# Performance work log

Measured on AMD Instinct MI355X. Metric: run time of the kernel, lower is better.

Reference implementation:

```python
import jax, jax.numpy as jnp
import numpy as np

N, T, J, NB = 2048, 81, 16, 15
D_ATT, HEADS, SEQ, D_LIN, NOISE = 48, 6, 31, 256, 45
BN_EPS, LN_EPS, SLOPE = 1e-5, 1e-6, 0.01

# Human3.6M 16-joint skeleton bone (parent, child) pairs
_BONES = [(0,1),(1,2),(2,3),(0,4),(4,5),(5,6),(0,7),(7,8),(8,9),(9,10),(8,11),(11,12),(12,13),(8,14),(14,15)]
BONES_P = np.array([p for p, c in _BONES])
BONES_C = np.array([c for p, c in _BONES])
_parent = {c: p for p, c in _BONES}
_bone_of = {c: i for i, (p, c) in enumerate(_BONES)}
_M = np.zeros((NB, J), np.float32)  # M[i,j]=1 iff bone i lies on root->joint j chain
for j in range(1, J):
    jj = j
    while jj != 0:
        _M[_bone_of[jj], j] = 1.0
        jj = _parent[jj]
M_BONE2POSE = jnp.asarray(_M)
FIXED_MASK = jnp.ones((NB,), jnp.float32).at[jnp.array([6, 7])].set(0.0)  # torso bones kept fixed


def _layer_norm(t, a, b):
    mean = t.mean(-1, keepdims=True)
    # torch.std default is unbiased (ddof=1); module divides by (std + eps)
    std = jnp.sqrt(((t - mean) ** 2).sum(-1, keepdims=True) / (t.shape[-1] - 1))
    return a * (t - mean) / (std + LN_EPS) + b


def _leaky(x):
    return jnp.where(x >= 0, x, SLOPE * x)


def _axis_angle_to_matrix(v):
    # Rodrigues: v (..., 3) axis-angle -> (..., 3, 3)
    theta = jnp.linalg.norm(v, axis=-1, keepdims=True)
    k = v / jnp.maximum(theta, 1e-8)
    c = jnp.cos(theta)[..., None]
    s = jnp.sin(theta)[..., None]
    kx, ky, kz = k[..., 0], k[..., 1], k[..., 2]
    z = jnp.zeros_like(kx)
    K = jnp.stack([jnp.stack([z, -kz, ky], -1),
                   jnp.stack([kz, z, -kx], -1),
                   jnp.stack([-ky, kx, z], -1)], -2)
    kk = k[..., :, None] * k[..., None, :]
    return c * jnp.eye(3, dtype=v.dtype) + s * K + (1 - c) * kk


def setup_inputs() -> dict:
    key = jax.random.key(0)
    ks = jax.random.split(key, 12)
    w = lambda k, shape, scale=0.05: jax.random.normal(k, shape, jnp.float32) * scale
    return {
        'inputs_3d': jax.random.normal(ks[0], (N, 1, T, J, 3), jnp.float32),
        'noise': jax.random.normal(ks[1], (N, NOISE), jnp.float32),
        'enc_w': w(ks[2], (D_ATT, 3)), 'enc_b': jnp.zeros((D_ATT,), jnp.float32),
        'enc_bn_g': jnp.ones((D_ATT,), jnp.float32), 'enc_bn_b': jnp.zeros((D_ATT,), jnp.float32),
        'ln_a': jnp.ones((D_ATT,), jnp.float32), 'ln_b': jnp.zeros((D_ATT,), jnp.float32),
        'wq': w(ks[3], (D_ATT, D_ATT)), 'bq': jnp.zeros((D_ATT,), jnp.float32),
        'wk': w(ks[4], (D_ATT, D_ATT)), 'bk': jnp.zeros((D_ATT,), jnp.float32),
        'wv': w(ks[5], (D_ATT, D_ATT)), 'bv': jnp.zeros((D_ATT,), jnp.float32),
        'wo': w(ks[6], (D_ATT, D_ATT)), 'bo': jnp.zeros((D_ATT,), jnp.float32),
        'w1': w(ks[7], (D_LIN, SEQ * D_ATT)), 'b1': jnp.zeros((D_LIN,), jnp.float32),
        'bn1_g': jnp.ones((D_LIN,), jnp.float32), 'bn1_b': jnp.zeros((D_LIN,), jnp.float32),
        'w2': w(ks[8], (NB * 4, D_LIN)), 'b2': w(ks[9], (NB * 4,), 0.1),
    }


def reference(inputs_3d, noise, enc_w, enc_b, enc_bn_g, enc_bn_b, ln_a, ln_b,
              wq, bq, wk, bk, wv, bv, wo, bo, w1, b1, bn1_g, bn1_b, w2, b2):
    x5 = inputs_3d[:, 0]                                  # (n, T, 16, 3)
    root = x5[:, :, :1, :]
    x = x5 - root                                         # root-centered
    bvec = x[..., BONES_C, :] - x[..., BONES_P, :]        # (n, T, 15, 3)
    blen = jnp.linalg.norm(bvec, axis=-1, keepdims=True)
    bunit = bvec / blen
    n, t_len = x.shape[0], x.shape[1]
    mid = (t_len - 1) // 2

    x_ = x[:, mid].reshape(n, -1)                         # (n, 48)
    y = jnp.concatenate([x_, noise], axis=-1).reshape(n, SEQ, 3)
    # Conv1d(k=1) == per-token linear; BatchNorm eval (running mean 0, var 1); Dropout off
    y = jax.nn.relu((y @ enc_w.T + enc_b) * enc_bn_g / jnp.sqrt(1.0 + BN_EPS) + enc_bn_b)

    # tiny 6-head self-attention with pre-LayerNorm and residual
    h = _layer_norm(y, ln_a, ln_b)
    d = D_ATT // HEADS
    q = (h @ wq.T + bq).reshape(n, SEQ, HEADS, d).transpose(0, 2, 1, 3)
    k = (h @ wk.T + bk).reshape(n, SEQ, HEADS, d).transpose(0, 2, 1, 3)
    v = (h @ wv.T + bv).reshape(n, SEQ, HEADS, d).transpose(0, 2, 1, 3)
    probs = jax.nn.softmax(jnp.einsum('nhqd,nhkd->nhqk', q, k) / (d ** 0.5), axis=-1)
    ctx = jnp.einsum('nhqk,nhkd->nhqd', probs, v).transpose(0, 2, 1, 3).reshape(n, SEQ, D_ATT)
    y = y + (ctx @ wo.T + bo)

    y = y.reshape(n, -1)                                  # (n, 1488)
    y = _leaky((y @ w1.T + b1) * bn1_g / jnp.sqrt(1.0 + BN_EPS) + bn1_b)
    y = _leaky(y @ w2.T + b2).reshape(n, NB, 4)           # (n, 15, 4)

    axis = y[..., :3]
    axis = axis / jnp.linalg.norm(axis, axis=-1, keepdims=True)
    theta = y[..., 3:4] / t_len                           # (n, 15, 1)
    t_idx = jnp.arange(t_len, dtype=y.dtype)              # (T,)
    vaa = axis[:, None] * (theta[:, None] * t_idx[None, :, None, None])  # (n, T, 15, 3)
    R = _axis_angle_to_matrix(vaa)                        # (n, T, 15, 3, 3)
    mod_unit = jnp.einsum('ntbij,ntbj->ntbi', R, bunit)
    mask = FIXED_MASK[None, None, :, None]
    mod_unit = mod_unit * mask + bunit * (1 - mask)
    ba_diff = 1 - jnp.sum(mod_unit * bunit, axis=-1)      # (n, T, 15)
    mod_bone = mod_unit * blen
    out = jnp.einsum('ntbc,bj->ntjc', mod_bone, M_BONE2POSE) + root  # (n, T, 16, 3)
    return out, ba_diff
```

## Files before the change

### kernel.cpp

```cpp
#include <hip/hip_runtime.h>
#include <math.h>

#define NS   2048
#define TL   81
#define NBN  15
#define DA   48
#define SQL  31
#define KD   1488
#define DL   256
#define MID  40

#define INV_SQRT_BN 0.99999500003749969f
#define SCALE_ATT   0.35355339059327373f

__global__ __launch_bounds__(256)
void attn_kernel(const float* __restrict__ x5, const float* __restrict__ noise,
                 const float* __restrict__ enc_w, const float* __restrict__ enc_b,
                 const float* __restrict__ enc_g, const float* __restrict__ enc_bb,
                 const float* __restrict__ ln_a, const float* __restrict__ ln_b,
                 const float* __restrict__ wq, const float* __restrict__ bq,
                 const float* __restrict__ wk, const float* __restrict__ bk,
                 const float* __restrict__ wv, const float* __restrict__ bv,
                 const float* __restrict__ wo, const float* __restrict__ bo,
                 float* __restrict__ y2)
{
    __shared__ float s93[96];
    __shared__ float sy[32*49];
    __shared__ float sh[32*49];
    __shared__ float sW[3*48*49];
    __shared__ __align__(16) float sQKV[32*148];
    __shared__ float smean[32], sinv[32];

    const int tid = threadIdx.x;
    const int n = blockIdx.x;

    if (tid < 93) {
        float v;
        if (tid < 48) {
            const float* base = x5 + ((size_t)n*TL + MID)*48;
            v = base[tid] - base[tid % 3];
        } else {
            v = noise[(size_t)n*45 + (tid-48)];
        }
        s93[tid] = v;
    }
    #pragma unroll
    for (int l=0; l<9; l++){
        int idx = tid + l*256;
        int f = idx/48, c = idx - f*48;
        int o = f*49 + c;
        sW[o]        = wq[idx];
        sW[2352 + o] = wk[idx];
        sW[4704 + o] = wv[idx];
    }
    __syncthreads();

    for (int idx=tid; idx<SQL*DA; idx+=256){
        int s = idx/48, f = idx - s*48;
        float a = enc_b[f]
                + s93[s*3+0]*enc_w[f*3+0]
                + s93[s*3+1]*enc_w[f*3+1]
                + s93[s*3+2]*enc_w[f*3+2];
        float v = a * (enc_g[f]*INV_SQRT_BN) + enc_bb[f];
        sy[s*49+f] = fmaxf(v, 0.0f);
    }
    __syncthreads();

    if (tid < SQL){
        float m = 0.f;
        for (int f=0; f<48; f++) m += sy[tid*49+f];
        m *= (1.0f/48.0f);
        float vs = 0.f;
        for (int f=0; f<48; f++){ float d = sy[tid*49+f]-m; vs += d*d; }
        float sd = sqrtf(vs * (1.0f/47.0f));
        smean[tid] = m;
        sinv[tid]  = 1.0f/(sd + 1e-6f);
    }
    __syncthreads();

    for (int idx=tid; idx<SQL*DA; idx+=256){
        int s = idx/48, f = idx - s*48;
        sh[s*49+f] = ln_a[f]*(sy[s*49+f]-smean[s])*sinv[s] + ln_b[f];
    }
    __syncthreads();

    if (tid < 192){
        const int sg = tid/24, fg = tid - (tid/24)*24;
        const int arr = fg >> 3;
        const int f0  = (fg & 7)*6;
        const float* wb = sW + arr*2352 + f0*49;
        const float* hb = sh + sg*4*49;
        float a0[6]={0,0,0,0,0,0}, a1[6]={0,0,0,0,0,0};
        float a2[6]={0,0,0,0,0,0}, a3[6]={0,0,0,0,0,0};
        for (int c=0; c<48; c++){
            float h0 = hb[c], h1 = hb[49+c], h2 = hb[98+c], h3 = hb[147+c];
            #pragma unroll
            for (int i=0;i<6;i++){
                float w = wb[i*49+c];
                a0[i] += h0*w; a1[i] += h1*w; a2[i] += h2*w; a3[i] += h3*w;
            }
        }
        const float* bias = (arr==0)? bq : (arr==1? bk : bv);
        #pragma unroll
        for (int i=0;i<6;i++){
            float b = bias[f0+i];
            int col = arr*48 + f0 + i;
            sQKV[(sg*4+0)*148 + col] = a0[i] + b;
            sQKV[(sg*4+1)*148 + col] = a1[i] + b;
            sQKV[(sg*4+2)*148 + col] = a2[i] + b;
            sQKV[(sg*4+3)*148 + col] = a3[i] + b;
        }
    }
    __syncthreads();

    #pragma unroll
    for (int l=0; l<9; l++){
        int idx = tid + l*256;
        sW[(idx/48)*49 + (idx%48)] = wo[idx];
    }
    if (tid < 186){
        const int hd = tid/31, qi = tid - (tid/31)*31;
        const float4 q0 = *(const float4*)(sQKV + qi*148 + hd*8);
        const float4 q1 = *(const float4*)(sQKV + qi*148 + hd*8 + 4);
        float sc[31]; float mx = -1e30f;
        for (int ki=0; ki<31; ki++){
            const float4 k0 = *(const float4*)(sQKV + ki*148 + 48 + hd*8);
            const float4 k1 = *(const float4*)(sQKV + ki*148 + 48 + hd*8 + 4);
            float d = q0.x*k0.x + q0.y*k0.y + q0.z*k0.z + q0.w*k0.w
                    + q1.x*k1.x + q1.y*k1.y + q1.z*k1.z + q1.w*k1.w;
            d *= SCALE_ATT;
            sc[ki] = d; mx = fmaxf(mx, d);
        }
        float ssum = 0.f;
        for (int ki=0; ki<31; ki++){ float e = expf(sc[ki]-mx); sc[ki]=e; ssum += e; }
        float rin = 1.0f/ssum;
        float4 c0 = {0,0,0,0}, c1 = {0,0,0,0};
        for (int ki=0; ki<31; ki++){
            float p = sc[ki];
            const float4 v0 = *(const float4*)(sQKV + ki*148 + 96 + hd*8);
            const float4 v1 = *(const float4*)(sQKV + ki*148 + 96 + hd*8 + 4);
            c0.x += p*v0.x; c0.y += p*v0.y; c0.z += p*v0.z; c0.w += p*v0.w;
            c1.x += p*v1.x; c1.y += p*v1.y; c1.z += p*v1.z; c1.w += p*v1.w;
        }
        float* cb = sh + qi*49 + hd*8;
        cb[0]=c0.x*rin; cb[1]=c0.y*rin; cb[2]=c0.z*rin; cb[3]=c0.w*rin;
        cb[4]=c1.x*rin; cb[5]=c1.y*rin; cb[6]=c1.z*rin; cb[7]=c1.w*rin;
    }
    __syncthreads();

    if (tid < 192){
        const int sg = tid/12, fg = tid - (tid/12)*12;
        const int f0 = fg*4;
        const float* wb = sW + f0*49;
        const float* cb = sh + sg*2*49;
        float a0[4]={0,0,0,0}, a1[4]={0,0,0,0};
        for (int c=0; c<48; c++){
            float x0 = cb[c], x1 = cb[49+c];
            #pragma unroll
            for (int i=0;i<4;i++){
                float w = wb[i*49+c];
                a0[i] += x0*w; a1[i] += x1*w;
            }
        }
        {
            int s = sg*2;
            if (s < 31){
                float* dst = y2 + (size_t)n*KD + s*48 + f0;
                const float* yb = sy + s*49 + f0;
                #pragma unroll
                for (int i=0;i<4;i++) dst[i] = yb[i] + a0[i] + bo[f0+i];
            }
        }
        {
            int s = sg*2+1;
            if (s < 31){
                float* dst = y2 + (size_t)n*KD + s*48 + f0;
                const float* yb = sy + s*49 + f0;
                #pragma unroll
                for (int i=0;i<4;i++) dst[i] = yb[i] + a1[i] + bo[f0+i];
            }
        }
    }
}

#define KSP 6
#define KPS 248
#define KCH 8

__global__ __launch_bounds__(256)
void gemm1_kernel(const float* __restrict__ y2, const float* __restrict__ w1,
                  float* __restrict__ y3raw, int use_partial)
{
    __shared__ __align__(16) float sB[KCH*256];
    __shared__ __align__(16) float sA[KCH*20];
    const int tid = threadIdx.x;
    const int bx = blockIdx.x;
    const int m0 = (bx & 127) * 16;
    const int split = bx >> 7;
    const int ks0 = split * KPS;
    const int c0 = (tid & 15)*4 + (tid >> 6)*64;
    const int r0 = ((tid >> 4) & 3)*4;

    const int bn = tid >> 1;
    const int bg = (tid & 1)*4;
    const int ar = tid >> 1;
    const int ag = (tid & 1)*4;

    float acc[4][4];
    #pragma unroll
    for (int i=0;i<4;i++)
        #pragma unroll
        for (int j=0;j<4;j++) acc[i][j]=0.f;

    for (int ch=0; ch<31; ch++){
        const int k0 = ks0 + ch*KCH;
        float4 b0v = *(const float4*)(w1 + (size_t)bn*KD        + k0 + bg);
        float4 b1v = *(const float4*)(w1 + (size_t)(bn+128)*KD  + k0 + bg);
        float4 av;
        if (tid < 32) av = *(const float4*)(y2 + (size_t)(m0+ar)*KD + k0 + ag);
        __syncthreads();
        sB[(bg+0)*256 + bn] = b0v.x;  sB[(bg+1)*256 + bn] = b0v.y;
        sB[(bg+2)*256 + bn] = b0v.z;  sB[(bg+3)*256 + bn] = b0v.w;
        sB[(bg+0)*256 + bn+128] = b1v.x;  sB[(bg+1)*256 + bn+128] = b1v.y;
        sB[(bg+2)*256 + bn+128] = b1v.z;  sB[(bg+3)*256 + bn+128] = b1v.w;
        if (tid < 32){
            sA[(ag+0)*20 + ar] = av.x;  sA[(ag+1)*20 + ar] = av.y;
            sA[(ag+2)*20 + ar] = av.z;  sA[(ag+3)*20 + ar] = av.w;
        }
        __syncthreads();
        #pragma unroll
        for (int kk=0; kk<KCH; kk++){
            float4 b = *(const float4*)(sB + kk*256 + c0);
            float4 a = *(const float4*)(sA + kk*20 + r0);
            acc[0][0] += a.x*b.x; acc[0][1] += a.x*b.y; acc[0][2] += a.x*b.z; acc[0][3] += a.x*b.w;
            acc[1][0] += a.y*b.x; acc[1][1] += a.y*b.y; acc[1][2] += a.y*b.z; acc[1][3] += a.y*b.w;
            acc[2][0] += a.z*b.x; acc[2][1] += a.z*b.y; acc[2][2] += a.z*b.z; acc[2][3] += a.z*b.w;
            acc[3][0] += a.w*b.x; acc[3][1] += a.w*b.y; acc[3][2] += a.w*b.z; acc[3][3] += a.w*b.w;
        }
    }

    if (use_partial){
        float* dst = y3raw + (size_t)split*NS*DL;
        #pragma unroll
        for (int i=0;i<4;i++){
            float4 v; v.x=acc[i][0]; v.y=acc[i][1]; v.z=acc[i][2]; v.w=acc[i][3];
            *(float4*)(dst + (size_t)(m0+r0+i)*DL + c0) = v;
        }
    } else {
        #pragma unroll
        for (int i=0;i<4;i++)
            #pragma unroll
            for (int j=0;j<4;j++)
                atomicAdd(y3raw + (size_t)(m0+r0+i)*DL + c0 + j, acc[i][j]);
    }
}

__global__ __launch_bounds__(256)
void head_kernel(const float* __restrict__ y3raw, const float* __restrict__ w2,
                 const float* __restrict__ b2, const float* __restrict__ b1,
                 const float* __restrict__ g1, const float* __restrict__ bb1,
                 float* __restrict__ at, int nsl)
{
    __shared__ float swc[64*60];
    __shared__ __align__(16) float sy3[16*256];
    __shared__ float sy4[16*61];
    const int tid = threadIdx.x;
    const int n0 = blockIdx.x * 16;

    #pragma unroll
    for (int l=0;l<4;l++){
        int idx = tid + l*256;
        int s = idx >> 6, i4 = (idx & 63) << 2;
        const float* src = y3raw + (size_t)(n0+s)*256 + i4;
        float4 v = *(const float4*)(src);
        if (nsl == 6){
            #pragma unroll
            for (int sl=1; sl<6; sl++){
                float4 p = *(const float4*)(src + (size_t)sl*NS*DL);
                v.x += p.x; v.y += p.y; v.z += p.z; v.w += p.w;
            }
        }
        const float4 vb = *(const float4*)(b1 + i4);
        const float4 vg = *(const float4*)(g1 + i4);
        const float4 vs = *(const float4*)(bb1 + i4);
        v.x = (v.x + vb.x)*(vg.x*INV_SQRT_BN) + vs.x;  v.x = v.x>=0.f? v.x : 0.01f*v.x;
        v.y = (v.y + vb.y)*(vg.y*INV_SQRT_BN) + vs.y;  v.y = v.y>=0.f? v.y : 0.01f*v.y;
        v.z = (v.z + vb.z)*(vg.z*INV_SQRT_BN) + vs.z;  v.z = v.z>=0.f? v.z : 0.01f*v.z;
        v.w = (v.w + vb.w)*(vg.w*INV_SQRT_BN) + vs.w;  v.w = v.w>=0.f? v.w : 0.01f*v.w;
        *(float4*)(sy3 + s*256 + i4) = v;
    }

    float acc[4]; int ss[4], mm[4];
    #pragma unroll
    for (int l=0;l<4;l++){
        int uu = tid + l*256;
        ss[l]=0; mm[l]=0; acc[l]=0.f;
        if (uu < 960){ ss[l]=uu/60; mm[l]=uu-ss[l]*60; acc[l]=b2[mm[l]]; }
    }

    for (int ch=0; ch<4; ch++){
        const int i0 = ch*64;
        __syncthreads();
        #pragma unroll
        for (int l=0;l<15;l++){
            int idx = tid + l*256;
            int m = idx >> 6, io = idx & 63;
            swc[io*60 + m] = w2[(size_t)m*256 + i0 + io];
        }
        __syncthreads();
        #pragma unroll
        for (int l=0;l<4;l++){
            int uu = tid + l*256;
            if (uu < 960){
                const float* yy = sy3 + ss[l]*256 + i0;
                float a = acc[l];
                #pragma unroll 8
                for (int io=0; io<64; io++) a += yy[io]*swc[io*60 + mm[l]];
                acc[l] = a;
            }
        }
    }
    __syncthreads();
    #pragma unroll
    for (int l=0;l<4;l++){
        int uu = tid + l*256;
        if (uu < 960){
            float a = acc[l];
            sy4[ss[l]*61 + mm[l]] = a>=0.f? a : 0.01f*a;
        }
    }
    __syncthreads();
    if (tid < 240){
        int s = tid/15, b = tid - s*15;
        const float* y4 = sy4 + s*61 + b*4;
        float ax=y4[0], ay=y4[1], az=y4[2], th=y4[3];
        float nr = sqrtf(ax*ax+ay*ay+az*az);
        float4 o;
        o.x = ax/nr; o.y = ay/nr; o.z = az/nr; o.w = th/81.0f;
        *(float4*)(at + (size_t)(n0+s)*60 + b*4) = o;
    }
}

__global__ __launch_bounds__(256)
void pose_kernel(const float* __restrict__ x5, const float* __restrict__ at,
                 float* __restrict__ out)
{
    const int gid = blockIdx.x*256 + threadIdx.x;
    if (gid >= NS*TL) return;
    const int n = gid / TL;
    const int t = gid - n*TL;
    const float ft = (float)t;

    float4 pv[12];
    {
        const float4* src = (const float4*)(x5 + (size_t)gid*48);
        #pragma unroll
        for (int i=0;i<12;i++) pv[i] = src[i];
    }
    float* p = (float*)pv;
    const float4* ab = (const float4*)(at + (size_t)n*60);

    float4 posv[12];
    float* pos = (float*)posv;
    pos[0]=p[0]; pos[1]=p[1]; pos[2]=p[2];
    float ba[15];

    const int PJ[15] = {0,1,2,0,4,5,0,7,8,9,8,11,12,8,14};
    const int CJ[15] = {1,2,3,4,5,6,7,8,9,10,11,12,13,14,15};

    #pragma unroll
    for (int b=0;b<15;b++){
        const int pj = PJ[b], cj = CJ[b];
        float bx = p[cj*3+0]-p[pj*3+0];
        float by = p[cj*3+1]-p[pj*3+1];
        float bz = p[cj*3+2]-p[pj*3+2];
        float bl = sqrtf(bx*bx+by*by+bz*bz);
        float ux = bx/bl, uy = by/bl, uz = bz/bl;
        float mx, my, mz;
        if (b==6 || b==7){
            mx=ux; my=uy; mz=uz;
        } else {
            float4 a = ab[b];
            float ang = a.w * ft;
            float cs = cosf(ang), sn = sinf(ang);
            float kd = a.x*ux + a.y*uy + a.z*uz;
            float cx = a.y*uz - a.z*uy;
            float cy = a.z*ux - a.x*uz;
            float cz = a.x*uy - a.y*ux;
            float oc = (1.0f-cs)*kd;
            mx = ux*cs + cx*sn + a.x*oc;
            my = uy*cs + cy*sn + a.y*oc;
            mz = uz*cs + cz*sn + a.z*oc;
        }
        ba[b] = 1.0f - (mx*ux+my*uy+mz*uz);
        pos[cj*3+0] = pos[pj*3+0] + mx*bl;
        pos[cj*3+1] = pos[pj*3+1] + my*bl;
        pos[cj*3+2] = pos[pj*3+2] + mz*bl;
    }

    {
        float4* dst = (float4*)(out + (size_t)gid*48);
        #pragma unroll
        for (int i=0;i<12;i++) dst[i] = posv[i];
    }
    {
        float* bd = out + (size_t)NS*TL*48 + (size_t)gid*15;
        #pragma unroll
        for (int b=0;b<15;b++) bd[b] = ba[b];
    }
}

extern "C" void kernel_launch(void* const* d_in, const int* in_sizes, int n_in,
                              void* d_out, int out_size, void* d_ws, size_t ws_size,
                              hipStream_t stream)
{
    const float* x5    = (const float*)d_in[0];
    const float* noise = (const float*)d_in[1];
    const float* enc_w = (const float*)d_in[2];
    const float* enc_b = (const float*)d_in[3];
    const float* enc_g = (const float*)d_in[4];
    const float* enc_bb= (const float*)d_in[5];
    const float* ln_a  = (const float*)d_in[6];
    const float* ln_b  = (const float*)d_in[7];
    const float* wq = (const float*)d_in[8];
    const float* bq = (const float*)d_in[9];
    const float* wk = (const float*)d_in[10];
    const float* bk = (const float*)d_in[11];
    const float* wv = (const float*)d_in[12];
    const float* bv = (const float*)d_in[13];
    const float* wo = (const float*)d_in[14];
    const float* bo = (const float*)d_in[15];
    const float* w1 = (const float*)d_in[16];
    const float* b1 = (const float*)d_in[17];
    const float* g1 = (const float*)d_in[18];
    const float* bb1= (const float*)d_in[19];
    const float* w2 = (const float*)d_in[20];
    const float* b2 = (const float*)d_in[21];
    float* out = (float*)d_out;

    float* ws = (float*)d_ws;
    float* y2 = ws;
    float* y3 = y2 + (size_t)NS*KD;

    const size_t need_partial = ((size_t)NS*KD + 6*(size_t)NS*DL + (size_t)NS*60) * 4;
    const int use_partial = (ws_size >= need_partial) ? 1 : 0;
    const int nsl = use_partial ? 6 : 1;
    float* at = y3 + (size_t)nsl*NS*DL;

    if (!use_partial)
        hipMemsetAsync(y3, 0, (size_t)NS*DL*sizeof(float), stream);

    attn_kernel<<<NS, 256, 0, stream>>>(x5, noise, enc_w, enc_b, enc_g, enc_bb,
                                        ln_a, ln_b, wq,bq,wk,bk,wv,bv,wo,bo, y2);
    gemm1_kernel<<<128*KSP, 256, 0, stream>>>(y2, w1, y3, use_partial);
    head_kernel<<<128, 256, 0, stream>>>(y3, w2, b2, b1, g1, bb1, at, nsl);
    pose_kernel<<<(NS*TL+255)/256, 256, 0, stream>>>(x5, at, out);

    (void)in_sizes; (void)n_in; (void)out_size;
}
```

Baseline: 252.2 us.

## Restructure attention kernel to one thread per token, reuse output buffer for partials

Rewrites the attention stage so each thread owns one sequence token, with two samples per 64-thread block. Encoding, layer norm and the Q/K/V/O projections now stay in registers, and only per-head K/V go through shared memory. Weights are read directly from global memory through the cache instead of being staged in shared memory. The split-K partial sums of the first GEMM are now always written into the output buffer as scratch, which drops the atomic fallback and the memset. The per-thread register arrays (y, h, o with 48 floats each) raise register pressure and may cause spills or low occupancy.

```diff
diff --git a/kernel.cpp b/kernel.cpp
--- a/kernel.cpp
+++ b/kernel.cpp
@@ -13,7 +13,7 @@
 #define INV_SQRT_BN 0.99999500003749969f
 #define SCALE_ATT   0.35355339059327373f
 
-__global__ __launch_bounds__(256)
+__global__ __launch_bounds__(64)
 void attn_kernel(const float* __restrict__ x5, const float* __restrict__ noise,
                  const float* __restrict__ enc_w, const float* __restrict__ enc_b,
                  const float* __restrict__ enc_g, const float* __restrict__ enc_bb,
@@ -24,161 +24,144 @@
                  const float* __restrict__ wo, const float* __restrict__ bo,
                  float* __restrict__ y2)
 {
-    __shared__ float s93[96];
-    __shared__ float sy[32*49];
-    __shared__ float sh[32*49];
-    __shared__ float sW[3*48*49];
-    __shared__ __align__(16) float sQKV[32*148];
-    __shared__ float smean[32], sinv[32];
-
-    const int tid = threadIdx.x;
-    const int n = blockIdx.x;
-
-    if (tid < 93) {
-        float v;
-        if (tid < 48) {
-            const float* base = x5 + ((size_t)n*TL + MID)*48;
-            v = base[tid] - base[tid % 3];
-        } else {
-            v = noise[(size_t)n*45 + (tid-48)];
-        }
-        s93[tid] = v;
-    }
-    #pragma unroll
-    for (int l=0; l<9; l++){
-        int idx = tid + l*256;
-        int f = idx/48, c = idx - f*48;
-        int o = f*49 + c;
-        sW[o]        = wq[idx];
-        sW[2352 + o] = wk[idx];
-        sW[4704 + o] = wv[idx];
-    }
-    __syncthreads();
-
-    for (int idx=tid; idx<SQL*DA; idx+=256){
-        int s = idx/48, f = idx - s*48;
-        float a = enc_b[f]
-                + s93[s*3+0]*enc_w[f*3+0]
-                + s93[s*3+1]*enc_w[f*3+1]
-                + s93[s*3+2]*enc_w[f*3+2];
-        float v = a * (enc_g[f]*INV_SQRT_BN) + enc_bb[f];
-        sy[s*49+f] = fmaxf(v, 0.0f);
-    }
-    __syncthreads();
-
-    if (tid < SQL){
-        float m = 0.f;
-        for (int f=0; f<48; f++) m += sy[tid*49+f];
-        m *= (1.0f/48.0f);
-        float vs = 0.f;
-        for (int f=0; f<48; f++){ float d = sy[tid*49+f]-m; vs += d*d; }
-        float sd = sqrtf(vs * (1.0f/47.0f));
-        smean[tid] = m;
-        sinv[tid]  = 1.0f/(sd + 1e-6f);
-    }
-    __syncthreads();
-
-    for (int idx=tid; idx<SQL*DA; idx+=256){
-        int s = idx/48, f = idx - s*48;
-        sh[s*49+f] = ln_a[f]*(sy[s*49+f]-smean[s])*sinv[s] + ln_b[f];
-    }
-    __syncthreads();
-
-    if (tid < 192){
-        const int sg = tid/24, fg = tid - (tid/24)*24;
-        const int arr = fg >> 3;
-        const int f0  = (fg & 7)*6;
-        const float* wb = sW + arr*2352 + f0*49;
-        const float* hb = sh + sg*4*49;
-        float a0[6]={0,0,0,0,0,0}, a1[6]={0,0,0,0,0,0};
-        float a2[6]={0,0,0,0,0,0}, a3[6]={0,0,0,0,0,0};
-        for (int c=0; c<48; c++){
-            float h0 = hb[c], h1 = hb[49+c], h2 = hb[98+c], h3 = hb[147+c];
+    __shared__ __align__(16) float sK[2*32*12];
+    __shared__ __align__(16) float sV[2*32*12];
+
+    const int lane = threadIdx.x;
+    const int smp  = lane >> 5;
+    const int s    = lane & 31;
+    const int scl  = (s < 31) ? s : 30;
+    const int n    = blockIdx.x*2 + smp;
+
+    float x0, x1, x2;
+    if (scl < 16){
+        const float* base = x5 + ((size_t)n*TL + MID)*48;
+        x0 = base[scl*3+0] - base[0];
+        x1 = base[scl*3+1] - base[1];
+        x2 = base[scl*3+2] - base[2];
+    } else {
+        const float* nb = noise + (size_t)n*45 + (scl*3 - 48);
+        x0 = nb[0]; x1 = nb[1]; x2 = nb[2];
+    }
+
+    float y[48];
+    #pragma unroll
+    for (int f=0; f<48; f++){
+        float a = enc_b[f] + x0*enc_w[f*3+0] + x1*enc_w[f*3+1] + x2*enc_w[f*3+2];
+        float v = a*(enc_g[f]*INV_SQRT_BN) + enc_bb[f];
+        y[f] = fmaxf(v, 0.0f);
+    }
+
+    float mean = 0.f;
+    #pragma unroll
+    for (int f=0; f<48; f++) mean += y[f];
+    mean *= (1.0f/48.0f);
+    float vs = 0.f;
+    #pragma unroll
+    for (int f=0; f<48; f++){ float d = y[f]-mean; vs += d*d; }
+    const float rstd = 1.0f/(sqrtf(vs*(1.0f/47.0f)) + 1e-6f);
+    float h[48];
+    #pragma unroll
+    for (int f=0; f<48; f++) h[f] = ln_a[f]*(y[f]-mean)*rstd + ln_b[f];
+
+    float o[48];
+    #pragma unroll
+    for (int f=0; f<48; f++) o[f] = 0.f;
+
+    #pragma unroll 1
+    for (int hd=0; hd<6; hd++){
+        const float* wqh = wq + hd*8*48;
+        const float* wkh = wk + hd*8*48;
+        const float* wvh = wv + hd*8*48;
+        float q8[8], k8[8], v8[8];
+        #pragma unroll
+        for (int j=0; j<8; j++){
+            q8[j] = bq[hd*8+j]; k8[j] = bk[hd*8+j]; v8[j] = bv[hd*8+j];
+        }
+        #pragma unroll
+        for (int j=0; j<8; j++){
+            const float* wqr = wqh + j*48;
+            const float* wkr = wkh + j*48;
+            const float* wvr = wvh + j*48;
+            float aq = q8[j], ak = k8[j], av = v8[j];
             #pragma unroll
-            for (int i=0;i<6;i++){
-                float w = wb[i*49+c];
-                a0[i] += h0*w; a1[i] += h1*w; a2[i] += h2*w; a3[i] += h3*w;
+            for (int c=0; c<48; c++){
+                float hc = h[c];
+                aq += hc*wqr[c];
+                ak += hc*wkr[c];
+                av += hc*wvr[c];
             }
-        }
-        const float* bias = (arr==0)? bq : (arr==1? bk : bv);
-        #pragma unroll
-        for (int i=0;i<6;i++){
-            float b = bias[f0+i];
-            int col = arr*48 + f0 + i;
-            sQKV[(sg*4+0)*148 + col] = a0[i] + b;
-            sQKV[(sg*4+1)*148 + col] = a1[i] + b;
-            sQKV[(sg*4+2)*148 + col] = a2[i] + b;
-            sQKV[(sg*4+3)*148 + col] = a3[i] + b;
-        }
-    }
-    __syncthreads();
-
-    #pragma unroll
-    for (int l=0; l<9; l++){
-        int idx = tid + l*256;
-        sW[(idx/48)*49 + (idx%48)] = wo[idx];
-    }
-    if (tid < 186){
-        const int hd = tid/31, qi = tid - (tid/31)*31;
-        const float4 q0 = *(const float4*)(sQKV + qi*148 + hd*8);
-        const float4 q1 = *(const float4*)(sQKV + qi*148 + hd*8 + 4);
-        float sc[31]; float mx = -1e30f;
+            q8[j] = aq; k8[j] = ak; v8[j] = av;
+        }
+
+        float* kr = sK + (smp*32+s)*12;
+        float* vr = sV + (smp*32+s)*12;
+        float4 t0, t1;
+        t0.x=k8[0]; t0.y=k8[1]; t0.z=k8[2]; t0.w=k8[3];
+        t1.x=k8[4]; t1.y=k8[5]; t1.z=k8[6]; t1.w=k8[7];
+        *(float4*)(kr) = t0; *(float4*)(kr+4) = t1;
+        t0.x=v8[0]; t0.y=v8[1]; t0.z=v8[2]; t0.w=v8[3];
+        t1.x=v8[4]; t1.y=v8[5]; t1.z=v8[6]; t1.w=v8[7];
+        *(float4*)(vr) = t0; *(float4*)(vr+4) = t1;
+        __syncthreads();
+
+        float sc[31];
+        float mx = -1e30f;
+        #pragma unroll
         for (int ki=0; ki<31; ki++){
-            const float4 k0 = *(const float4*)(sQKV + ki*148 + 48 + hd*8);
-            const float4 k1 = *(const float4*)(sQKV + ki*148 + 48 + hd*8 + 4);
-            float d = q0.x*k0.x + q0.y*k0.y + q0.z*k0.z + q0.w*k0.w
-                    + q1.x*k1.x + q1.y*k1.y + q1.z*k1.z + q1.w*k1.w;
+            const float* kp = sK + (smp*32+ki)*12;
+            float4 ka = *(const float4*)(kp);
+            float4 kb = *(const float4*)(kp+4);
+            float d = q8[0]*ka.x + q8[1]*ka.y + q8[2]*ka.z + q8[3]*ka.w
+                    + q8[4]*kb.x + q8[5]*kb.y + q8[6]*kb.z + q8[7]*kb.w;
             d *= SCALE_ATT;
-            sc[ki] = d; mx = fmaxf(mx, d);
+            sc[ki] = d;
+            mx = fmaxf(mx, d);
         }
         float ssum = 0.f;
-        for (int ki=0; ki<31; ki++){ float e = expf(sc[ki]-mx); sc[ki]=e; ssum += e; }
-        float rin = 1.0f/ssum;
-        float4 c0 = {0,0,0,0}, c1 = {0,0,0,0};
+        #pragma unroll
         for (int ki=0; ki<31; ki++){
+            float e = __expf(sc[ki]-mx);
+            sc[ki] = e; ssum += e;
+        }
+        const float rin = 1.0f/ssum;
+
+        float c8[8];
+        #pragma unroll
+        for (int j=0; j<8; j++) c8[j] = 0.f;
+        #pragma unroll
+        for (int ki=0; ki<31; ki++){
+            const float* vp = sV + (smp*32+ki)*12;
+            float4 va = *(const float4*)(vp);
+            float4 vb = *(const float4*)(vp+4);
             float p = sc[ki];
-            const float4 v0 = *(const float4*)(sQKV + ki*148 + 96 + hd*8);
-            const float4 v1 = *(const float4*)(sQKV + ki*148 + 96 + hd*8 + 4);
-            c0.x += p*v0.x; c0.y += p*v0.y; c0.z += p*v0.z; c0.w += p*v0.w;
-            c1.x += p*v1.x; c1.y += p*v1.y; c1.z += p*v1.z; c1.w += p*v1.w;
-        }
-        float* cb = sh + qi*49 + hd*8;
-        cb[0]=c0.x*rin; cb[1]=c0.y*rin; cb[2]=c0.z*rin; cb[3]=c0.w*rin;
-        cb[4]=c1.x*rin; cb[5]=c1.y*rin; cb[6]=c1.z*rin; cb[7]=c1.w*rin;
-    }
-    __syncthreads();
-
-    if (tid < 192){
-        const int sg = tid/12, fg = tid - (tid/12)*12;
-        const int f0 = fg*4;
-        const float* wb = sW + f0*49;
-        const float* cb = sh + sg*2*49;
-        float a0[4]={0,0,0,0}, a1[4]={0,0,0,0};
-        for (int c=0; c<48; c++){
-            float x0 = cb[c], x1 = cb[49+c];
+            c8[0] += p*va.x; c8[1] += p*va.y; c8[2] += p*va.z; c8[3] += p*va.w;
+            c8[4] += p*vb.x; c8[5] += p*vb.y; c8[6] += p*vb.z; c8[7] += p*vb.w;
+        }
+        #pragma unroll
+        for (int j=0; j<8; j++) c8[j] *= rin;
+
+        #pragma unroll
+        for (int f=0; f<48; f++){
+            const float* wor = wo + f*48 + hd*8;
+            float a = o[f];
             #pragma unroll
-            for (int i=0;i<4;i++){
-                float w = wb[i*49+c];
-                a0[i] += x0*w; a1[i] += x1*w;
-            }
-        }
-        {
-            int s = sg*2;
-            if (s < 31){
-                float* dst = y2 + (size_t)n*KD + s*48 + f0;
-                const float* yb = sy + s*49 + f0;
-                #pragma unroll
-                for (int i=0;i<4;i++) dst[i] = yb[i] + a0[i] + bo[f0+i];
-            }
-        }
-        {
-            int s = sg*2+1;
-            if (s < 31){
-                float* dst = y2 + (size_t)n*KD + s*48 + f0;
-                const float* yb = sy + s*49 + f0;
-                #pragma unroll
-                for (int i=0;i<4;i++) dst[i] = yb[i] + a1[i] + bo[f0+i];
-            }
+            for (int j=0; j<8; j++) a += c8[j]*wor[j];
+            o[f] = a;
+        }
+        __syncthreads();
+    }
+
+    if (s < 31){
+        float* dst = y2 + (size_t)n*KD + s*48;
+        #pragma unroll
+        for (int f4=0; f4<12; f4++){
+            float4 v;
+            v.x = y[f4*4+0] + o[f4*4+0] + bo[f4*4+0];
+            v.y = y[f4*4+1] + o[f4*4+1] + bo[f4*4+1];
+            v.z = y[f4*4+2] + o[f4*4+2] + bo[f4*4+2];
+            v.w = y[f4*4+3] + o[f4*4+3] + bo[f4*4+3];
+            *(float4*)(dst + f4*4) = v;
         }
     }
 }
@@ -189,7 +172,7 @@
 
 __global__ __launch_bounds__(256)
 void gemm1_kernel(const float* __restrict__ y2, const float* __restrict__ w1,
-                  float* __restrict__ y3raw, int use_partial)
+                  float* __restrict__ y3p)
 {
     __shared__ __align__(16) float sB[KCH*256];
     __shared__ __align__(16) float sA[KCH*20];
@@ -239,27 +222,19 @@
         }
     }
 
-    if (use_partial){
-        float* dst = y3raw + (size_t)split*NS*DL;
-        #pragma unroll
-        for (int i=0;i<4;i++){
-            float4 v; v.x=acc[i][0]; v.y=acc[i][1]; v.z=acc[i][2]; v.w=acc[i][3];
-            *(float4*)(dst + (size_t)(m0+r0+i)*DL + c0) = v;
-        }
-    } else {
-        #pragma unroll
-        for (int i=0;i<4;i++)
-            #pragma unroll
-            for (int j=0;j<4;j++)
-                atomicAdd(y3raw + (size_t)(m0+r0+i)*DL + c0 + j, acc[i][j]);
+    float* dst = y3p + (size_t)split*NS*DL;
+    #pragma unroll
+    for (int i=0;i<4;i++){
+        float4 v; v.x=acc[i][0]; v.y=acc[i][1]; v.z=acc[i][2]; v.w=acc[i][3];
+        *(float4*)(dst + (size_t)(m0+r0+i)*DL + c0) = v;
     }
 }
 
 __global__ __launch_bounds__(256)
-void head_kernel(const float* __restrict__ y3raw, const float* __restrict__ w2,
+void head_kernel(const float* __restrict__ y3p, const float* __restrict__ w2,
                  const float* __restrict__ b2, const float* __restrict__ b1,
                  const float* __restrict__ g1, const float* __restrict__ bb1,
-                 float* __restrict__ at, int nsl)
+                 float* __restrict__ at)
 {
     __shared__ float swc[64*60];
     __shared__ __align__(16) float sy3[16*256];
@@ -271,22 +246,20 @@
     for (int l=0;l<4;l++){
         int idx = tid + l*256;
         int s = idx >> 6, i4 = (idx & 63) << 2;
-        const float* src = y3raw + (size_t)(n0+s)*256 + i4;
+        const float* src = y3p + (size_t)(n0+s)*256 + i4;
         float4 v = *(const float4*)(src);
-        if (nsl == 6){
-            #pragma unroll
-            for (int sl=1; sl<6; sl++){
-                float4 p = *(const float4*)(src + (size_t)sl*NS*DL);
-                v.x += p.x; v.y += p.y; v.z += p.z; v.w += p.w;
-            }
+        #pragma unroll
+        for (int sl=1; sl<6; sl++){
+            float4 p = *(const float4*)(src + (size_t)sl*NS*DL);
+            v.x += p.x; v.y += p.y; v.z += p.z; v.w += p.w;
         }
         const float4 vb = *(const float4*)(b1 + i4);
         const float4 vg = *(const float4*)(g1 + i4);
-        const float4 vs = *(const float4*)(bb1 + i4);
-        v.x = (v.x + vb.x)*(vg.x*INV_SQRT_BN) + vs.x;  v.x = v.x>=0.f? v.x : 0.01f*v.x;
-        v.y = (v.y + vb.y)*(vg.y*INV_SQRT_BN) + vs.y;  v.y = v.y>=0.f? v.y : 0.01f*v.y;
-        v.z = (v.z + vb.z)*(vg.z*INV_SQRT_BN) + vs.z;  v.z = v.z>=0.f? v.z : 0.01f*v.z;
-        v.w = (v.w + vb.w)*(vg.w*INV_SQRT_BN) + vs.w;  v.w = v.w>=0.f? v.w : 0.01f*v.w;
+        const float4 vsb = *(const float4*)(bb1 + i4);
+        v.x = (v.x + vb.x)*(vg.x*INV_SQRT_BN) + vsb.x;  v.x = v.x>=0.f? v.x : 0.01f*v.x;
+        v.y = (v.y + vb.y)*(vg.y*INV_SQRT_BN) + vsb.y;  v.y = v.y>=0.f? v.y : 0.01f*v.y;
+        v.z = (v.z + vb.z)*(vg.z*INV_SQRT_BN) + vsb.z;  v.z = v.z>=0.f? v.z : 0.01f*v.z;
+        v.w = (v.w + vb.w)*(vg.w*INV_SQRT_BN) + vsb.w;  v.w = v.w>=0.f? v.w : 0.01f*v.w;
         *(float4*)(sy3 + s*256 + i4) = v;
     }
 
@@ -440,21 +413,14 @@
 
     float* ws = (float*)d_ws;
     float* y2 = ws;
-    float* y3 = y2 + (size_t)NS*KD;
-
-    const size_t need_partial = ((size_t)NS*KD + 6*(size_t)NS*DL + (size_t)NS*60) * 4;
-    const int use_partial = (ws_size >= need_partial) ? 1 : 0;
-    const int nsl = use_partial ? 6 : 1;
-    float* at = y3 + (size_t)nsl*NS*DL;
-
-    if (!use_partial)
-        hipMemsetAsync(y3, 0, (size_t)NS*DL*sizeof(float), stream);
-
-    attn_kernel<<<NS, 256, 0, stream>>>(x5, noise, enc_w, enc_b, enc_g, enc_bb,
-                                        ln_a, ln_b, wq,bq,wk,bk,wv,bv,wo,bo, y2);
-    gemm1_kernel<<<128*KSP, 256, 0, stream>>>(y2, w1, y3, use_partial);
-    head_kernel<<<128, 256, 0, stream>>>(y3, w2, b2, b1, g1, bb1, at, nsl);
+    float* at = y2 + (size_t)NS*KD;
+    float* y3p = out;
+
+    attn_kernel<<<NS/2, 64, 0, stream>>>(x5, noise, enc_w, enc_b, enc_g, enc_bb,
+                                         ln_a, ln_b, wq,bq,wk,bk,wv,bv,wo,bo, y2);
+    gemm1_kernel<<<128*KSP, 256, 0, stream>>>(y2, w1, y3p);
+    head_kernel<<<128, 256, 0, stream>>>(y3p, w2, b2, b1, g1, bb1, at);
     pose_kernel<<<(NS*TL+255)/256, 256, 0, stream>>>(x5, at, out);
 
-    (void)in_sizes; (void)n_in; (void)out_size;
+    (void)in_sizes; (void)n_in; (void)out_size; (void)ws_size;
 }
```

Measured after the change: 362.3 us. +43.7%, slower.
